# Kernel optimization log

Hardware: AMD Instinct MI355X
Metric: run time of the kernel (lower is better)

## Reference

```python
import jax, jax.numpy as jnp
import numpy as np

B, S, I, Hd = 128, 512, 128, 512


def setup_inputs() -> dict:
    key = jax.random.key(0)
    ks = jax.random.split(key, 6)
    s_i = 1.0 / np.sqrt(I)
    s_h = 1.0 / np.sqrt(Hd)
    return {
        "x": jax.random.normal(ks[0], (B, S, I), jnp.float32),
        "w_emb": jax.random.uniform(ks[1], (Hd, I), jnp.float32, -s_i, s_i),
        "b_emb": jax.random.uniform(ks[2], (Hd,), jnp.float32, -s_i, s_i),
        "w_ih": jax.random.uniform(ks[3], (3 * Hd, Hd), jnp.float32, -s_h, s_h),
        "b_ih": jax.random.uniform(ks[4], (3 * Hd,), jnp.float32, -s_h, s_h),
        "b_hh": jax.random.uniform(ks[5], (3 * Hd,), jnp.float32, -s_h, s_h),
    }


def reference(x, w_emb, b_emb, w_ih, b_ih, b_hh):
    # Original loop runs one GRU step per timestep with hidden state reset to
    # zero every call, so every step is independent -> fully batched over time.
    # With h=0 the recurrent matmul W_hh @ h vanishes; only b_hh survives.
    emb = jnp.einsum('bsi,hi->bsh', x, w_emb) + b_emb          # [B,S,Hd]
    gi = jnp.einsum('bsh,gh->bsg', emb, w_ih) + b_ih           # [B,S,3Hd]
    ir, iz, inn = jnp.split(gi, 3, axis=-1)
    b_hr, b_hz, b_hn = jnp.split(b_hh, 3)
    r = jax.nn.sigmoid(ir + b_hr)
    z = jax.nn.sigmoid(iz + b_hz)
    n = jnp.tanh(inn + r * b_hn)
    h = (1.0 - z) * n                                          # h' = (1-z)*n + z*0
    H = h[:, :-1, :]               # [B, S-1, Hd]
    h_last = h[:, -1, :][None]     # [1, B, Hd] (num_layers*dirs = 1)
    return (H, h_last)
```

## Files before the change

### kernel.cpp

```cpp
#include <hip/hip_runtime.h>
#include <hip/hip_bf16.h>
#include <stdint.h>

#define M_TOT   65536
#define I_DIM   128
#define HD      512
#define HOFF    33488896
#define HROW    261632

typedef __bf16 bf16x8 __attribute__((ext_vector_type(8)));
typedef float f32x4 __attribute__((ext_vector_type(4)));

struct __align__(8) bf16x4_t { __hip_bfloat16 v[4]; };

__device__ __forceinline__ void async_load16(const void* g, void* l) {
  __builtin_amdgcn_global_load_lds(
      (const __attribute__((address_space(1))) void*)g,
      (__attribute__((address_space(3))) void*)l, 16, 0, 0);
}

__device__ __forceinline__ float fastrcp(float x) {
  return __builtin_amdgcn_rcpf(x);
}
__device__ __forceinline__ float sigf(float x) {
  return fastrcp(1.0f + __expf(-x));
}
__device__ __forceinline__ float tanhfast(float x) {
  return 1.0f - 2.0f * fastrcp(__expf(2.0f * x) + 1.0f);
}

#define PB_X   8192
#define PB_WI  768
#define PB_TR  16
#define PB_BF  384
__global__ void prep(const float* __restrict__ x,
                     const float* __restrict__ we,
                     const float* __restrict__ wi,
                     const float* __restrict__ b_emb,
                     const float* __restrict__ b_ih,
                     __hip_bfloat16* __restrict__ xb,
                     __hip_bfloat16* __restrict__ weT,
                     __hip_bfloat16* __restrict__ wib,
                     float* __restrict__ bfu) {
  const int bid = blockIdx.x;
  const int tid = threadIdx.x;
  if (bid < PB_X) {
    const int i = bid * 256 + tid;
    const float4 v = ((const float4*)x)[i];
    bf16x4_t o;
    o.v[0] = __float2bfloat16(v.x); o.v[1] = __float2bfloat16(v.y);
    o.v[2] = __float2bfloat16(v.z); o.v[3] = __float2bfloat16(v.w);
    ((bf16x4_t*)xb)[i] = o;
  } else if (bid < PB_X + PB_WI) {
    const int i = (bid - PB_X) * 256 + tid;
    const float4 v = ((const float4*)wi)[i];
    bf16x4_t o;
    o.v[0] = __float2bfloat16(v.x); o.v[1] = __float2bfloat16(v.y);
    o.v[2] = __float2bfloat16(v.z); o.v[3] = __float2bfloat16(v.w);
    ((bf16x4_t*)wib)[i] = o;
  } else if (bid < PB_X + PB_WI + PB_TR) {
    const int b = bid - (PB_X + PB_WI);
    const int i  = b * 8 + (tid >> 5);
    const int h0 = (tid & 31) * 16;
    bf16x8 v0, v1;
#pragma unroll
    for (int j = 0; j < 8; ++j) {
      v0[j] = (__bf16)we[(size_t)(h0 + j) * I_DIM + i];
      v1[j] = (__bf16)we[(size_t)(h0 + 8 + j) * I_DIM + i];
    }
    *(bf16x8*)&weT[(size_t)i * HD + h0] = v0;
    *(bf16x8*)&weT[(size_t)i * HD + h0 + 8] = v1;
  } else {
    const int g = (bid - (PB_X + PB_WI + PB_TR)) * 4 + (tid >> 6);
    const int lane = tid & 63;
    const float4* row = (const float4*)(wi + (size_t)g * HD);
    const float4* be  = (const float4*)b_emb;
    float s = 0.0f;
#pragma unroll
    for (int j = 0; j < 2; ++j) {
      const float4 a = row[lane * 2 + j];
      const float4 b = be[lane * 2 + j];
      s += a.x * b.x + a.y * b.y + a.z * b.z + a.w * b.w;
    }
#pragma unroll
    for (int off = 32; off > 0; off >>= 1) s += __shfl_down(s, off);
    if (lane == 0) bfu[g] = s + b_ih[g];
  }
}

__global__ __launch_bounds__(256, 2) void fuse_gemm(
    const __hip_bfloat16* __restrict__ wib,
    const __hip_bfloat16* __restrict__ weT,
    __hip_bfloat16* __restrict__ wf)
{
  __shared__ __align__(16) __hip_bfloat16 smem[32768];

  const int tid  = threadIdx.x;
  const int w    = tid >> 6;
  const int lane = tid & 63;
  const int g0 = blockIdx.x * 128;
  const int wm = (w >> 1) * 64;
  const int wn = (w & 1) * 64;
  const int lrow = lane >> 3;
  const int gc   = ((lane & 7) ^ lrow) * 8;
  const int l15 = lane & 15;
  const int q   = lane >> 4;
  const int sx  = l15 & 7;

  f32x4 acc[4][4];
#pragma unroll
  for (int i = 0; i < 4; ++i)
#pragma unroll
    for (int j = 0; j < 4; ++j) acc[i][j] = (f32x4)0.0f;

#pragma unroll
  for (int c = 0; c < 4; ++c) {
    const int chunk = w * 4 + c;
    const int row = chunk * 8 + lrow;
    async_load16(wib + (size_t)(g0 + row) * HD + gc, (void*)&smem[chunk * 512]);
    async_load16(weT + (size_t)row * HD + gc, (void*)&smem[8192 + chunk * 512]);
  }
  __syncthreads();

#pragma unroll
  for (int t = 0; t < 8; ++t) {
    const __hip_bfloat16* As = smem + (t & 1) * 16384;
    const __hip_bfloat16* Bs = As + 8192;
    if (t < 7) {
      __hip_bfloat16* An = smem + ((t + 1) & 1) * 16384;
      const int k = (t + 1) * 64;
#pragma unroll
      for (int c = 0; c < 4; ++c) {
        const int chunk = w * 4 + c;
        const int row = chunk * 8 + lrow;
        async_load16(wib + (size_t)(g0 + row) * HD + k + gc, (void*)&An[chunk * 512]);
        async_load16(weT + (size_t)row * HD + k + gc, (void*)&An[8192 + chunk * 512]);
      }
    }
    __builtin_amdgcn_sched_barrier(0);
#pragma unroll
    for (int ks = 0; ks < 2; ++ks) {
      const int s = ((ks * 4 + q) ^ sx) * 8;
      bf16x8 af[4], bfr[4];
#pragma unroll
      for (int mi = 0; mi < 4; ++mi)
        af[mi] = *(const bf16x8*)&As[(wm + mi * 16 + l15) * 64 + s];
#pragma unroll
      for (int ni = 0; ni < 4; ++ni)
        bfr[ni] = *(const bf16x8*)&Bs[(wn + ni * 16 + l15) * 64 + s];
      __builtin_amdgcn_s_setprio(1);
#pragma unroll
      for (int ni = 0; ni < 4; ++ni)
#pragma unroll
        for (int mi = 0; mi < 4; ++mi)
          acc[mi][ni] = __builtin_amdgcn_mfma_f32_16x16x32_bf16(
              af[mi], bfr[ni], acc[mi][ni], 0, 0, 0);
      __builtin_amdgcn_s_setprio(0);
    }
    if (t < 7) __syncthreads();
  }

  __hip_bfloat16* ebuf = &smem[w * 4096];
#pragma unroll
  for (int ni = 0; ni < 4; ++ni)
#pragma unroll
    for (int mi = 0; mi < 4; ++mi)
#pragma unroll
      for (int r = 0; r < 4; ++r)
        ebuf[(mi * 16 + q * 4 + r) * 64 + ni * 16 + l15] =
            __float2bfloat16(acc[mi][ni][r]);
#pragma unroll
  for (int i = 0; i < 8; ++i) {
    const int row  = i * 8 + (lane >> 3);
    const int colb = (lane & 7) * 8;
    const bf16x8 v = *(const bf16x8*)&ebuf[row * 64 + colb];
    *(bf16x8*)&wf[(size_t)(g0 + wm + row) * I_DIM + wn + colb] = v;
  }
}

__device__ __forceinline__ void stage_B32(const __hip_bfloat16* __restrict__ wf,
                                          int hc, char* Bbuf,
                                          int w, int lrow, int gc) {
  const int h0 = hc * 32;
#pragma unroll
  for (int j = 0; j < 6; ++j) {
    const int idx = w * 6 + j;
    const int kh = idx / 12;
    const int cr = idx % 12;
    const int r  = cr * 8 + lrow;
    const int g  = r >> 5;
    const int hh = r & 31;
    async_load16(wf + (size_t)(g * HD + h0 + hh) * I_DIM + kh * 64 + gc,
                 (void*)&((__hip_bfloat16*)Bbuf)[kh * 6144 + cr * 512]);
  }
}

__global__ __launch_bounds__(256, 2) void gru_main(
    const __hip_bfloat16* __restrict__ xb,
    const __hip_bfloat16* __restrict__ wf,
    const float* __restrict__ bfu,
    const float* __restrict__ b_hh,
    float* __restrict__ out)
{
  __shared__ __align__(16) char smem[81920];
  __hip_bfloat16* A0 = (__hip_bfloat16*)smem;

  const int tid  = threadIdx.x;
  const int w    = tid >> 6;
  const int lane = tid & 63;
  const int m0 = blockIdx.x * 128;
  const int wm = w * 32;
  const int lrow = lane >> 3;
  const int gc   = ((lane & 7) ^ lrow) * 8;
  const int l15 = lane & 15;
  const int q   = lane >> 4;
  const int sx  = l15 & 7;

#pragma unroll
  for (int kh = 0; kh < 2; ++kh)
#pragma unroll
    for (int c = 0; c < 4; ++c) {
      const int chunk = w * 4 + c;
      async_load16(xb + (size_t)(m0 + chunk * 8 + lrow) * I_DIM + kh * 64 + gc,
                   (void*)&A0[kh * 8192 + chunk * 512]);
    }
  stage_B32(wf, 0, smem + 32768, w, lrow, gc);
  __syncthreads();

  bf16x8 af[4][2];
#pragma unroll
  for (int ks = 0; ks < 4; ++ks) {
    const int half = ks >> 1;
    const int s = (((ks & 1) * 4 + q) ^ sx) * 8;
#pragma unroll
    for (int mi = 0; mi < 2; ++mi)
      af[ks][mi] = *(const bf16x8*)&A0[half * 8192 + (wm + mi * 16 + l15) * 64 + s];
  }
  __syncthreads();

  float* obuf = (float*)(smem + w * 8192);
  const int srow = lane >> 3;
  const int scol = (lane & 7) * 4;

#pragma unroll 2
  for (int hc = 0; hc < 16; ++hc) {
    const __hip_bfloat16* Bs =
        (const __hip_bfloat16*)(smem + 32768 + (hc & 1) * 24576);
    if (hc < 15)
      stage_B32(wf, hc + 1, smem + 32768 + ((hc + 1) & 1) * 24576, w, lrow, gc);
    __builtin_amdgcn_sched_barrier(0);

    f32x4 acc[3][2][2];
#pragma unroll
    for (int g = 0; g < 3; ++g)
#pragma unroll
      for (int mi = 0; mi < 2; ++mi)
#pragma unroll
        for (int ni = 0; ni < 2; ++ni) acc[g][mi][ni] = (f32x4)0.0f;

    __builtin_amdgcn_s_setprio(1);
#pragma unroll
    for (int g = 0; g < 3; ++g)
#pragma unroll
      for (int ks = 0; ks < 4; ++ks) {
        const int half = ks >> 1;
        const int s = (((ks & 1) * 4 + q) ^ sx) * 8;
#pragma unroll
        for (int ni = 0; ni < 2; ++ni) {
          const bf16x8 bv =
              *(const bf16x8*)&Bs[half * 6144 + (g * 32 + ni * 16 + l15) * 64 + s];
#pragma unroll
          for (int mi = 0; mi < 2; ++mi)
            acc[g][mi][ni] = __builtin_amdgcn_mfma_f32_16x16x32_bf16(
                af[ks][mi], bv, acc[g][mi][ni], 0, 0, 0);
        }
      }
    __builtin_amdgcn_s_setprio(0);

    const int h0 = hc * 32;
#pragma unroll
    for (int ni = 0; ni < 2; ++ni) {
      const int col = h0 + ni * 16 + l15;
      const float br = bfu[col] + b_hh[col];
      const float bz = bfu[HD + col] + b_hh[HD + col];
      const float bn = bfu[2 * HD + col];
      const float bhn = b_hh[2 * HD + col];
#pragma unroll
      for (int mi = 0; mi < 2; ++mi) {
#pragma unroll
        for (int r = 0; r < 4; ++r) {
          const float rr = sigf(acc[0][mi][ni][r] + br);
          const float zz = sigf(acc[1][mi][ni][r] + bz);
          const float nn = tanhfast(acc[2][mi][ni][r] + bn + rr * bhn);
          obuf[(mi * 16 + q * 4 + r) * 40 + ni * 16 + l15] = (1.0f - zz) * nn;
        }
      }
    }
#pragma unroll
    for (int i = 0; i < 4; ++i) {
      const int row = i * 8 + srow;
      const float4 v = *(const float4*)&obuf[row * 40 + scol];
      const int m = m0 + wm + row;
      const int b = m >> 9;
      const int s = m & 511;
      float* dst = (s < 511)
          ? out + (size_t)b * HROW + (size_t)s * HD + h0 + scol
          : out + (size_t)HOFF + (size_t)b * HD + h0 + scol;
      *(float4*)dst = v;
    }
    __syncthreads();
  }
}

extern "C" void kernel_launch(void* const* d_in, const int* in_sizes, int n_in,
                              void* d_out, int out_size, void* d_ws, size_t ws_size,
                              hipStream_t stream) {
  const float* x_f     = (const float*)d_in[0];
  const float* w_emb_f = (const float*)d_in[1];
  const float* b_emb   = (const float*)d_in[2];
  const float* w_ih_f  = (const float*)d_in[3];
  const float* b_ih    = (const float*)d_in[4];
  const float* b_hh    = (const float*)d_in[5];
  float* out = (float*)d_out;

  char* ws = (char*)d_ws;
  __hip_bfloat16* x_bf   = (__hip_bfloat16*)(ws);
  __hip_bfloat16* wi_bf  = (__hip_bfloat16*)(ws + 16777216);
  __hip_bfloat16* weT_bf = (__hip_bfloat16*)(ws + 18350080);
  __hip_bfloat16* wf_bf  = (__hip_bfloat16*)(ws + 18481152);
  float*          b_fu   = (float*)(ws + 18874368);

  prep<<<PB_X + PB_WI + PB_TR + PB_BF, 256, 0, stream>>>(
      x_f, w_emb_f, w_ih_f, b_emb, b_ih, x_bf, weT_bf, wi_bf, b_fu);

  fuse_gemm<<<12, 256, 0, stream>>>(wi_bf, weT_bf, wf_bf);

  gru_main<<<M_TOT / 128, 256, 0, stream>>>(x_bf, wf_bf, b_fu, b_hh, out);
}
```

Baseline: 209.4 us.

## Fold x bf16 conversion into main GEMM and fuse weight prep into one kernel

Drops the separate pass that converted x to bf16 in workspace. The main kernel now reads fp32 x directly into registers and converts it there, which removes a full read/write round trip of x. The weight-fusion GEMM (W_ih·W_emb) and the bias fold are merged into a single fp32 scalar kernel, so three launches become two. The shared-memory staging of outputs is also removed in favour of direct scalar stores, which cuts LDS use but gives less coalesced global writes and a scalar fp32 prep GEMM.

```diff
diff --git a/kernel.cpp b/kernel.cpp
--- a/kernel.cpp
+++ b/kernel.cpp
@@ -11,8 +11,6 @@
 typedef __bf16 bf16x8 __attribute__((ext_vector_type(8)));
 typedef float f32x4 __attribute__((ext_vector_type(4)));
 
-struct __align__(8) bf16x4_t { __hip_bfloat16 v[4]; };
-
 __device__ __forceinline__ void async_load16(const void* g, void* l) {
   __builtin_amdgcn_global_load_lds(
       (const __attribute__((address_space(1))) void*)g,
@@ -29,152 +27,53 @@
   return 1.0f - 2.0f * fastrcp(__expf(2.0f * x) + 1.0f);
 }
 
-#define PB_X   8192
-#define PB_WI  768
-#define PB_TR  16
-#define PB_BF  384
-__global__ void prep(const float* __restrict__ x,
-                     const float* __restrict__ we,
-                     const float* __restrict__ wi,
-                     const float* __restrict__ b_emb,
-                     const float* __restrict__ b_ih,
-                     __hip_bfloat16* __restrict__ xb,
-                     __hip_bfloat16* __restrict__ weT,
-                     __hip_bfloat16* __restrict__ wib,
-                     float* __restrict__ bfu) {
-  const int bid = blockIdx.x;
+__global__ __launch_bounds__(256) void wprep(
+    const float* __restrict__ wi,
+    const float* __restrict__ we,
+    const float* __restrict__ b_emb,
+    const float* __restrict__ b_ih,
+    __hip_bfloat16* __restrict__ wf,
+    float* __restrict__ bfu)
+{
+  __shared__ float wis[4 * 512];
+  __shared__ float bes[512];
   const int tid = threadIdx.x;
-  if (bid < PB_X) {
-    const int i = bid * 256 + tid;
-    const float4 v = ((const float4*)x)[i];
-    bf16x4_t o;
-    o.v[0] = __float2bfloat16(v.x); o.v[1] = __float2bfloat16(v.y);
-    o.v[2] = __float2bfloat16(v.z); o.v[3] = __float2bfloat16(v.w);
-    ((bf16x4_t*)xb)[i] = o;
-  } else if (bid < PB_X + PB_WI) {
-    const int i = (bid - PB_X) * 256 + tid;
-    const float4 v = ((const float4*)wi)[i];
-    bf16x4_t o;
-    o.v[0] = __float2bfloat16(v.x); o.v[1] = __float2bfloat16(v.y);
-    o.v[2] = __float2bfloat16(v.z); o.v[3] = __float2bfloat16(v.w);
-    ((bf16x4_t*)wib)[i] = o;
-  } else if (bid < PB_X + PB_WI + PB_TR) {
-    const int b = bid - (PB_X + PB_WI);
-    const int i  = b * 8 + (tid >> 5);
-    const int h0 = (tid & 31) * 16;
-    bf16x8 v0, v1;
-#pragma unroll
-    for (int j = 0; j < 8; ++j) {
-      v0[j] = (__bf16)we[(size_t)(h0 + j) * I_DIM + i];
-      v1[j] = (__bf16)we[(size_t)(h0 + 8 + j) * I_DIM + i];
-    }
-    *(bf16x8*)&weT[(size_t)i * HD + h0] = v0;
-    *(bf16x8*)&weT[(size_t)i * HD + h0 + 8] = v1;
-  } else {
-    const int g = (bid - (PB_X + PB_WI + PB_TR)) * 4 + (tid >> 6);
-    const int lane = tid & 63;
-    const float4* row = (const float4*)(wi + (size_t)g * HD);
-    const float4* be  = (const float4*)b_emb;
-    float s = 0.0f;
-#pragma unroll
-    for (int j = 0; j < 2; ++j) {
-      const float4 a = row[lane * 2 + j];
-      const float4 b = be[lane * 2 + j];
-      s += a.x * b.x + a.y * b.y + a.z * b.z + a.w * b.w;
-    }
-#pragma unroll
-    for (int off = 32; off > 0; off >>= 1) s += __shfl_down(s, off);
-    if (lane == 0) bfu[g] = s + b_ih[g];
-  }
-}
-
-__global__ __launch_bounds__(256, 2) void fuse_gemm(
-    const __hip_bfloat16* __restrict__ wib,
-    const __hip_bfloat16* __restrict__ weT,
-    __hip_bfloat16* __restrict__ wf)
-{
-  __shared__ __align__(16) __hip_bfloat16 smem[32768];
-
-  const int tid  = threadIdx.x;
-  const int w    = tid >> 6;
-  const int lane = tid & 63;
-  const int g0 = blockIdx.x * 128;
-  const int wm = (w >> 1) * 64;
-  const int wn = (w & 1) * 64;
-  const int lrow = lane >> 3;
-  const int gc   = ((lane & 7) ^ lrow) * 8;
-  const int l15 = lane & 15;
-  const int q   = lane >> 4;
-  const int sx  = l15 & 7;
-
-  f32x4 acc[4][4];
-#pragma unroll
-  for (int i = 0; i < 4; ++i)
-#pragma unroll
-    for (int j = 0; j < 4; ++j) acc[i][j] = (f32x4)0.0f;
-
-#pragma unroll
-  for (int c = 0; c < 4; ++c) {
-    const int chunk = w * 4 + c;
-    const int row = chunk * 8 + lrow;
-    async_load16(wib + (size_t)(g0 + row) * HD + gc, (void*)&smem[chunk * 512]);
-    async_load16(weT + (size_t)row * HD + gc, (void*)&smem[8192 + chunk * 512]);
-  }
+  const int g0  = blockIdx.x * 4;
+
+#pragma unroll
+  for (int j = 0; j < 2; ++j)
+    ((float4*)wis)[j * 256 + tid] =
+        ((const float4*)(wi + (size_t)g0 * HD))[j * 256 + tid];
+  if (tid < 128) ((float4*)bes)[tid] = ((const float4*)b_emb)[tid];
   __syncthreads();
 
-#pragma unroll
-  for (int t = 0; t < 8; ++t) {
-    const __hip_bfloat16* As = smem + (t & 1) * 16384;
-    const __hip_bfloat16* Bs = As + 8192;
-    if (t < 7) {
-      __hip_bfloat16* An = smem + ((t + 1) & 1) * 16384;
-      const int k = (t + 1) * 64;
-#pragma unroll
-      for (int c = 0; c < 4; ++c) {
-        const int chunk = w * 4 + c;
-        const int row = chunk * 8 + lrow;
-        async_load16(wib + (size_t)(g0 + row) * HD + k + gc, (void*)&An[chunk * 512]);
-        async_load16(weT + (size_t)row * HD + k + gc, (void*)&An[8192 + chunk * 512]);
-      }
-    }
-    __builtin_amdgcn_sched_barrier(0);
-#pragma unroll
-    for (int ks = 0; ks < 2; ++ks) {
-      const int s = ((ks * 4 + q) ^ sx) * 8;
-      bf16x8 af[4], bfr[4];
-#pragma unroll
-      for (int mi = 0; mi < 4; ++mi)
-        af[mi] = *(const bf16x8*)&As[(wm + mi * 16 + l15) * 64 + s];
-#pragma unroll
-      for (int ni = 0; ni < 4; ++ni)
-        bfr[ni] = *(const bf16x8*)&Bs[(wn + ni * 16 + l15) * 64 + s];
-      __builtin_amdgcn_s_setprio(1);
-#pragma unroll
-      for (int ni = 0; ni < 4; ++ni)
-#pragma unroll
-        for (int mi = 0; mi < 4; ++mi)
-          acc[mi][ni] = __builtin_amdgcn_mfma_f32_16x16x32_bf16(
-              af[mi], bfr[ni], acc[mi][ni], 0, 0, 0);
-      __builtin_amdgcn_s_setprio(0);
-    }
-    if (t < 7) __syncthreads();
-  }
-
-  __hip_bfloat16* ebuf = &smem[w * 4096];
-#pragma unroll
-  for (int ni = 0; ni < 4; ++ni)
-#pragma unroll
-    for (int mi = 0; mi < 4; ++mi)
-#pragma unroll
-      for (int r = 0; r < 4; ++r)
-        ebuf[(mi * 16 + q * 4 + r) * 64 + ni * 16 + l15] =
-            __float2bfloat16(acc[mi][ni][r]);
-#pragma unroll
-  for (int i = 0; i < 8; ++i) {
-    const int row  = i * 8 + (lane >> 3);
-    const int colb = (lane & 7) * 8;
-    const bf16x8 v = *(const bf16x8*)&ebuf[row * 64 + colb];
-    *(bf16x8*)&wf[(size_t)(g0 + wm + row) * I_DIM + wn + colb] = v;
+  const int i   = tid & 127;
+  const int seg = tid >> 7;
+  float a0 = 0.0f, a1 = 0.0f;
+#pragma unroll 4
+  for (int h = 0; h < 512; h += 4) {
+    const f32x4 w0 = *(const f32x4*)&wis[(seg * 2 + 0) * 512 + h];
+    const f32x4 w1 = *(const f32x4*)&wis[(seg * 2 + 1) * 512 + h];
+#pragma unroll
+    for (int j = 0; j < 4; ++j) {
+      const float wev = we[(size_t)(h + j) * I_DIM + i];
+      a0 = fmaf(w0[j], wev, a0);
+      a1 = fmaf(w1[j], wev, a1);
+    }
+  }
+  wf[(size_t)(g0 + seg * 2 + 0) * I_DIM + i] = __float2bfloat16(a0);
+  wf[(size_t)(g0 + seg * 2 + 1) * I_DIM + i] = __float2bfloat16(a1);
+
+  if (tid < 64) {
+#pragma unroll
+    for (int g = 0; g < 4; ++g) {
+      float s = 0.0f;
+#pragma unroll
+      for (int h = 0; h < 8; ++h) s += wis[g * 512 + tid + h * 64] * bes[tid + h * 64];
+#pragma unroll
+      for (int off = 32; off; off >>= 1) s += __shfl_down(s, off);
+      if (tid == 0) bfu[g0 + g] = s + b_ih[g0 + g];
+    }
   }
 }
 
@@ -196,14 +95,13 @@
 }
 
 __global__ __launch_bounds__(256, 2) void gru_main(
-    const __hip_bfloat16* __restrict__ xb,
+    const float* __restrict__ x_f,
     const __hip_bfloat16* __restrict__ wf,
     const float* __restrict__ bfu,
     const float* __restrict__ b_hh,
     float* __restrict__ out)
 {
-  __shared__ __align__(16) char smem[81920];
-  __hip_bfloat16* A0 = (__hip_bfloat16*)smem;
+  __shared__ __align__(16) char smem[49152];
 
   const int tid  = threadIdx.x;
   const int w    = tid >> 6;
@@ -216,38 +114,31 @@
   const int q   = lane >> 4;
   const int sx  = l15 & 7;
 
-#pragma unroll
-  for (int kh = 0; kh < 2; ++kh)
-#pragma unroll
-    for (int c = 0; c < 4; ++c) {
-      const int chunk = w * 4 + c;
-      async_load16(xb + (size_t)(m0 + chunk * 8 + lrow) * I_DIM + kh * 64 + gc,
-                   (void*)&A0[kh * 8192 + chunk * 512]);
-    }
-  stage_B32(wf, 0, smem + 32768, w, lrow, gc);
+  stage_B32(wf, 0, smem, w, lrow, gc);
+
+  bf16x8 af[4][2];
+#pragma unroll
+  for (int mi = 0; mi < 2; ++mi) {
+    const float* xp = x_f + (size_t)(m0 + wm + mi * 16 + l15) * I_DIM + q * 8;
+#pragma unroll
+    for (int ks = 0; ks < 4; ++ks) {
+      const float4 c0 = *(const float4*)(xp + ks * 32);
+      const float4 c1 = *(const float4*)(xp + ks * 32 + 4);
+      bf16x8 v;
+      v[0] = (__bf16)c0.x; v[1] = (__bf16)c0.y;
+      v[2] = (__bf16)c0.z; v[3] = (__bf16)c0.w;
+      v[4] = (__bf16)c1.x; v[5] = (__bf16)c1.y;
+      v[6] = (__bf16)c1.z; v[7] = (__bf16)c1.w;
+      af[ks][mi] = v;
+    }
+  }
   __syncthreads();
-
-  bf16x8 af[4][2];
-#pragma unroll
-  for (int ks = 0; ks < 4; ++ks) {
-    const int half = ks >> 1;
-    const int s = (((ks & 1) * 4 + q) ^ sx) * 8;
-#pragma unroll
-    for (int mi = 0; mi < 2; ++mi)
-      af[ks][mi] = *(const bf16x8*)&A0[half * 8192 + (wm + mi * 16 + l15) * 64 + s];
-  }
-  __syncthreads();
-
-  float* obuf = (float*)(smem + w * 8192);
-  const int srow = lane >> 3;
-  const int scol = (lane & 7) * 4;
 
 #pragma unroll 2
   for (int hc = 0; hc < 16; ++hc) {
-    const __hip_bfloat16* Bs =
-        (const __hip_bfloat16*)(smem + 32768 + (hc & 1) * 24576);
+    const __hip_bfloat16* Bs = (const __hip_bfloat16*)(smem + (hc & 1) * 24576);
     if (hc < 15)
-      stage_B32(wf, hc + 1, smem + 32768 + ((hc + 1) & 1) * 24576, w, lrow, gc);
+      stage_B32(wf, hc + 1, smem + ((hc + 1) & 1) * 24576, w, lrow, gc);
     __builtin_amdgcn_sched_barrier(0);
 
     f32x4 acc[3][2][2];
@@ -287,26 +178,22 @@
       const float bhn = b_hh[2 * HD + col];
 #pragma unroll
       for (int mi = 0; mi < 2; ++mi) {
+        const int mbase = m0 + wm + mi * 16 + q * 4;
 #pragma unroll
         for (int r = 0; r < 4; ++r) {
           const float rr = sigf(acc[0][mi][ni][r] + br);
           const float zz = sigf(acc[1][mi][ni][r] + bz);
           const float nn = tanhfast(acc[2][mi][ni][r] + bn + rr * bhn);
-          obuf[(mi * 16 + q * 4 + r) * 40 + ni * 16 + l15] = (1.0f - zz) * nn;
+          const float hv = (1.0f - zz) * nn;
+          const int m = mbase + r;
+          const int b = m >> 9;
+          const int s = m & 511;
+          float* dst = (s < 511)
+              ? out + (size_t)b * HROW + (size_t)s * HD + col
+              : out + (size_t)HOFF + (size_t)b * HD + col;
+          *dst = hv;
         }
       }
-    }
-#pragma unroll
-    for (int i = 0; i < 4; ++i) {
-      const int row = i * 8 + srow;
-      const float4 v = *(const float4*)&obuf[row * 40 + scol];
-      const int m = m0 + wm + row;
-      const int b = m >> 9;
-      const int s = m & 511;
-      float* dst = (s < 511)
-          ? out + (size_t)b * HROW + (size_t)s * HD + h0 + scol
-          : out + (size_t)HOFF + (size_t)b * HD + h0 + scol;
-      *(float4*)dst = v;
     }
     __syncthreads();
   }
@@ -324,16 +211,10 @@
   float* out = (float*)d_out;
 
   char* ws = (char*)d_ws;
-  __hip_bfloat16* x_bf   = (__hip_bfloat16*)(ws);
-  __hip_bfloat16* wi_bf  = (__hip_bfloat16*)(ws + 16777216);
-  __hip_bfloat16* weT_bf = (__hip_bfloat16*)(ws + 18350080);
-  __hip_bfloat16* wf_bf  = (__hip_bfloat16*)(ws + 18481152);
-  float*          b_fu   = (float*)(ws + 18874368);
-
-  prep<<<PB_X + PB_WI + PB_TR + PB_BF, 256, 0, stream>>>(
-      x_f, w_emb_f, w_ih_f, b_emb, b_ih, x_bf, weT_bf, wi_bf, b_fu);
-
-  fuse_gemm<<<12, 256, 0, stream>>>(wi_bf, weT_bf, wf_bf);
-
-  gru_main<<<M_TOT / 128, 256, 0, stream>>>(x_bf, wf_bf, b_fu, b_hh, out);
-}
+  __hip_bfloat16* wf_bf = (__hip_bfloat16*)(ws);
+  float*          b_fu  = (float*)(ws + 393216);
+
+  wprep<<<384, 256, 0, stream>>>(w_ih_f, w_emb_f, b_emb, b_ih, wf_bf, b_fu);
+
+  gru_main<<<M_TOT / 128, 256, 0, stream>>>(x_f, wf_bf, b_fu, b_hh, out);
+}
```

Result: no change. 213.1 us (+1.8%).
